# Kernel optimization log

Hardware: AMD Instinct MI355X
Metric: run time of the kernel (lower is better)

## Reference

```python
import jax, jax.numpy as jnp
import numpy as np

LN_EPS = 1e-5  # torch LayerNorm default


def layer_norm(x, g, b):
    m = jnp.mean(x, axis=-1, keepdims=True)
    v = jnp.mean((x - m) ** 2, axis=-1, keepdims=True)
    return (x - m) / jnp.sqrt(v + LN_EPS) * g + b


def scatter_mean(src, idx, n):
    # src: [E, h], idx: [E] -> [n, h], mean with count clamped to >= 1
    s = jax.ops.segment_sum(src, idx, num_segments=n)
    cnt = jax.ops.segment_sum(jnp.ones((src.shape[0],), src.dtype), idx, num_segments=n)
    return s / jnp.clip(cnt, 1.0)[:, None]


def setup_inputs() -> dict:
    key = jax.random.key(0)
    ks = jax.random.split(key, 16)
    N, C, E, h = 200000, 50000, 600000, 128

    def w(k, shape, fan_in):
        return (jax.random.normal(k, shape, jnp.float32) / np.float32(np.sqrt(fan_in)))

    ci = jax.random.randint(ks[2], (E,), 0, C)
    vi = jax.random.randint(ks[3], (E,), 0, N)
    return {
        "vh": jax.random.normal(ks[0], (N, h), jnp.float32),
        "ch": jax.random.normal(ks[1], (C, h), jnp.float32),
        "edge_index": jnp.stack([ci, vi]).astype(jnp.int64),
        "ew": jax.random.normal(ks[4], (E,), jnp.float32),
        "v2c_lin_w": w(ks[5], (h, h), h), "v2c_lin_b": jnp.zeros((h,), jnp.float32),
        "v2c_gate_w": w(ks[6], (h, 1), 1), "v2c_gate_b": jnp.zeros((h,), jnp.float32),
        "v2c_upd_w": w(ks[7], (h, 2 * h), 2 * h), "v2c_upd_b": jnp.zeros((h,), jnp.float32),
        "v2c_ln_g": jnp.ones((h,), jnp.float32), "v2c_ln_b": jnp.zeros((h,), jnp.float32),
        "c2v_lin_w": w(ks[8], (h, h), h), "c2v_lin_b": jnp.zeros((h,), jnp.float32),
        "c2v_gate_w": w(ks[9], (h, 1), 1), "c2v_gate_b": jnp.zeros((h,), jnp.float32),
        "c2v_upd_w": w(ks[10], (h, 2 * h), 2 * h), "c2v_upd_b": jnp.zeros((h,), jnp.float32),
        "c2v_ln_g": jnp.ones((h,), jnp.float32), "c2v_ln_b": jnp.zeros((h,), jnp.float32),
    }


def reference(vh, ch, edge_index, ew,
              v2c_lin_w, v2c_lin_b, v2c_gate_w, v2c_gate_b,
              v2c_upd_w, v2c_upd_b, v2c_ln_g, v2c_ln_b,
              c2v_lin_w, c2v_lin_b, c2v_gate_w, c2v_gate_b,
              c2v_upd_w, c2v_upd_b, c2v_ln_g, c2v_ln_b):
    ci, vi = edge_index[0], edge_index[1]
    e = ew[:, None]  # [E, 1]

    # var -> con
    gate = jax.nn.sigmoid(e @ v2c_gate_w.T + v2c_gate_b)          # [E, h]
    msg = (vh @ v2c_lin_w.T + v2c_lin_b)[vi] * gate               # gather + gate
    agg = scatter_mean(msg, ci, ch.shape[0])                      # [C, h]
    ch_new = jax.nn.relu(layer_norm(
        jnp.concatenate([agg, ch], -1) @ v2c_upd_w.T + v2c_upd_b,
        v2c_ln_g, v2c_ln_b))

    # con -> var (uses updated ch)
    gate = jax.nn.sigmoid(e @ c2v_gate_w.T + c2v_gate_b)
    msg = (ch_new @ c2v_lin_w.T + c2v_lin_b)[ci] * gate
    agg = scatter_mean(msg, vi, vh.shape[0])                      # [N, h]
    vh_new = jax.nn.relu(layer_norm(
        jnp.concatenate([agg, vh], -1) @ c2v_upd_w.T + c2v_upd_b,
        c2v_ln_g, c2v_ln_b))

    return vh_new, ch_new
```

## Files before the change

### kernel.cpp

```cpp
#include <hip/hip_runtime.h>

#define LN_EPS 1e-5f

typedef float f32x4 __attribute__((ext_vector_type(4)));
typedef short bf16x8 __attribute__((ext_vector_type(8)));
typedef unsigned short u16x4 __attribute__((ext_vector_type(4)));

__device__ __forceinline__ unsigned short f2bf(float f) {
  unsigned int u = __float_as_uint(f);
  u = (u + 0x7fffu + ((u >> 16) & 1u)) >> 16;
  return (unsigned short)u;
}
__device__ __forceinline__ float bf2f(unsigned short h) {
  return __uint_as_float((unsigned int)h << 16);
}
__device__ __forceinline__ float sigm(float x) {
  return 1.f / (1.f + __expf(-x));
}

__global__ __launch_bounds__(256) void cvt_hist(const float* __restrict__ wa,
                                                const float* __restrict__ wb,
                                                const float* __restrict__ wc,
                                                const float* __restrict__ wd,
                                                unsigned short* __restrict__ oa,
                                                unsigned short* __restrict__ ob,
                                                unsigned short* __restrict__ oc,
                                                unsigned short* __restrict__ od,
                                                const int* __restrict__ ci,
                                                const int* __restrict__ vi,
                                                int* __restrict__ cntC,
                                                int* __restrict__ cntV,
                                                int* __restrict__ rankC,
                                                int* __restrict__ rankV, int E, int hgrid) {
  if ((int)blockIdx.x < 384) {
    int i = blockIdx.x * 256 + threadIdx.x;
    if (i < 16384) oa[i] = f2bf(wa[i]);
    else if (i < 49152) ob[i - 16384] = f2bf(wb[i - 16384]);
    else if (i < 65536) oc[i - 49152] = f2bf(wc[i - 49152]);
    else if (i < 98304) od[i - 65536] = f2bf(wd[i - 65536]);
    return;
  }
  int hb = blockIdx.x - 384;
  int tid = hb * 256 + threadIdx.x;
  int T = hgrid * 256;
  int e[4], c[4], v[4];
  bool ok[4];
#pragma unroll
  for (int i = 0; i < 4; ++i) {
    e[i] = tid + i * T;
    ok[i] = e[i] < E;
  }
#pragma unroll
  for (int i = 0; i < 4; ++i) if (ok[i]) c[i] = ci[e[i]];
#pragma unroll
  for (int i = 0; i < 4; ++i) if (ok[i]) v[i] = vi[e[i]];
  int rc[4], rv[4];
#pragma unroll
  for (int i = 0; i < 4; ++i) if (ok[i]) rc[i] = atomicAdd(&cntC[c[i]], 1);
#pragma unroll
  for (int i = 0; i < 4; ++i) if (ok[i]) rv[i] = atomicAdd(&cntV[v[i]], 1);
#pragma unroll
  for (int i = 0; i < 4; ++i) if (ok[i]) rankC[e[i]] = rc[i];
#pragma unroll
  for (int i = 0; i < 4; ++i) if (ok[i]) rankV[e[i]] = rv[i];
}

__device__ __forceinline__ void scan1_body(const int* __restrict__ cnt,
                                           int* __restrict__ off,
                                           int* __restrict__ bsum, int M, int bid,
                                           int* s) {
  int base = bid * 1024 + threadIdx.x * 4;
  int v[4];
  int tot = 0;
#pragma unroll
  for (int i = 0; i < 4; ++i) {
    int idx = base + i;
    v[i] = (idx < M) ? cnt[idx] : 0;
    tot += v[i];
  }
  s[threadIdx.x] = tot;
  __syncthreads();
  for (int d = 1; d < 256; d <<= 1) {
    int t = (threadIdx.x >= d) ? s[threadIdx.x - d] : 0;
    __syncthreads();
    s[threadIdx.x] += t;
    __syncthreads();
  }
  int excl = s[threadIdx.x] - tot;
#pragma unroll
  for (int i = 0; i < 4; ++i) {
    int idx = base + i;
    if (idx < M) off[idx] = excl;
    excl += v[i];
  }
  if (threadIdx.x == 255) bsum[bid] = s[255];
}

__global__ __launch_bounds__(256) void scanA(const int* __restrict__ cntC,
                                             int* __restrict__ offC,
                                             int* __restrict__ bsC, int Mc,
                                             const int* __restrict__ cntV,
                                             int* __restrict__ offV,
                                             int* __restrict__ bsV, int Mv, int nbC) {
  __shared__ int s[256];
  if ((int)blockIdx.x < nbC)
    scan1_body(cntC, offC, bsC, Mc, blockIdx.x, s);
  else
    scan1_body(cntV, offV, bsV, Mv, blockIdx.x - nbC, s);
}

__global__ __launch_bounds__(256) void scanB(int* __restrict__ bsC, int nbC,
                                             int* __restrict__ bsV, int nbV) {
  __shared__ int s[256];
  __shared__ int carry;
  int* bsum = (blockIdx.x == 0) ? bsC : bsV;
  int nb = (blockIdx.x == 0) ? nbC : nbV;
  if (threadIdx.x == 0) carry = 0;
  __syncthreads();
  for (int base = 0; base < nb; base += 256) {
    int idx = base + threadIdx.x;
    int v = (idx < nb) ? bsum[idx] : 0;
    s[threadIdx.x] = v;
    __syncthreads();
    for (int d = 1; d < 256; d <<= 1) {
      int t = (threadIdx.x >= d) ? s[threadIdx.x - d] : 0;
      __syncthreads();
      s[threadIdx.x] += t;
      __syncthreads();
    }
    if (idx < nb) bsum[idx] = s[threadIdx.x] - v + carry;
    __syncthreads();
    if (threadIdx.x == 0) carry += s[255];
    __syncthreads();
  }
}

__global__ __launch_bounds__(256) void scanC(int* __restrict__ offC,
                                             const int* __restrict__ bsC, int Mc,
                                             int* __restrict__ offV,
                                             const int* __restrict__ bsV, int Mv,
                                             int E, int gC) {
  if ((int)blockIdx.x < gC) {
    int idx = blockIdx.x * 256 + threadIdx.x;
    if (idx < Mc) offC[idx] += bsC[idx >> 10];
    if (idx == Mc) offC[Mc] = E;
  } else {
    int idx = (blockIdx.x - gC) * 256 + threadIdx.x;
    if (idx < Mv) offV[idx] += bsV[idx >> 10];
    if (idx == Mv) offV[Mv] = E;
  }
}

__global__ __launch_bounds__(512) void lin_scatter(
    const float* __restrict__ X, const unsigned short* __restrict__ Wbf,
    const float* __restrict__ bias, unsigned short* __restrict__ out,
    unsigned short* __restrict__ bfdst, int M,
    const int* __restrict__ ci, const int* __restrict__ vi,
    const float* __restrict__ ew, const int* __restrict__ offC,
    const int* __restrict__ offV, const int* __restrict__ rankC,
    const int* __restrict__ rankV, int2* __restrict__ edataC,
    int2* __restrict__ edataV, int E, int sgrid) {
  __shared__ unsigned short Bs[128][136];
  const int tid = threadIdx.x;
  const int bid = blockIdx.x;
  const int s3 = 3 * sgrid;

  bool isScatter;
  int sidx = 0, lidx;
  if (bid < s3) {
    if (bid % 3 == 0) {
      isScatter = true;
      sidx = bid / 3;
    } else {
      isScatter = false;
      lidx = bid - bid / 3 - 1;
    }
  } else {
    isScatter = false;
    lidx = bid - sgrid;
  }

  if (isScatter) {
    int gtid = sidx * 512 + tid;
    int T = sgrid * 512;
    int e[2], c[2], v[2], wb[2], rc[2], rv[2];
    bool ok[2];
#pragma unroll
    for (int i = 0; i < 2; ++i) {
      e[i] = gtid + i * T;
      ok[i] = e[i] < E;
    }
#pragma unroll
    for (int i = 0; i < 2; ++i) if (ok[i]) c[i] = ci[e[i]];
#pragma unroll
    for (int i = 0; i < 2; ++i) if (ok[i]) v[i] = vi[e[i]];
#pragma unroll
    for (int i = 0; i < 2; ++i) if (ok[i]) wb[i] = __float_as_int(ew[e[i]]);
#pragma unroll
    for (int i = 0; i < 2; ++i) if (ok[i]) rc[i] = rankC[e[i]];
#pragma unroll
    for (int i = 0; i < 2; ++i) if (ok[i]) rv[i] = rankV[e[i]];
#pragma unroll
    for (int i = 0; i < 2; ++i) if (ok[i]) edataC[offC[c[i]] + rc[i]] = make_int2(v[i], wb[i]);
#pragma unroll
    for (int i = 0; i < 2; ++i) if (ok[i]) edataV[offV[v[i]] + rv[i]] = make_int2(c[i], wb[i]);
    return;
  }

  const int lane = tid & 63, wv = tid >> 6;
  const int lr = lane & 15, lg = lane >> 4;
  const int row0 = lidx * 128 + wv * 16;
  const int arow = row0 + lr;
  const bool rowok = arow < M;
  const float* xrow = X + (size_t)arow * 128;

  float4 x0[4], x1[4];
#pragma unroll
  for (int ks = 0; ks < 4; ++ks) {
    int kb = ks * 32 + lg * 8;
    if (rowok) {
      x0[ks] = *reinterpret_cast<const float4*>(xrow + kb);
      x1[ks] = *reinterpret_cast<const float4*>(xrow + kb + 4);
    } else {
      x0[ks] = make_float4(0.f, 0.f, 0.f, 0.f);
      x1[ks] = x0[ks];
    }
  }

#pragma unroll
  for (int it = 0; it < 4; ++it) {
    int q = tid + it * 512;
    int n = q >> 4, kq = (q & 15) * 8;
    *reinterpret_cast<bf16x8*>(&Bs[n][kq]) =
        *reinterpret_cast<const bf16x8*>(&Wbf[(size_t)n * 128 + kq]);
  }

  bf16x8 a[4];
#pragma unroll
  for (int ks = 0; ks < 4; ++ks) {
    a[ks] = (bf16x8){(short)f2bf(x0[ks].x), (short)f2bf(x0[ks].y),
                     (short)f2bf(x0[ks].z), (short)f2bf(x0[ks].w),
                     (short)f2bf(x1[ks].x), (short)f2bf(x1[ks].y),
                     (short)f2bf(x1[ks].z), (short)f2bf(x1[ks].w)};
    if (rowok)
      *reinterpret_cast<bf16x8*>(&bfdst[(size_t)arow * 256 + 128 + ks * 32 + lg * 8]) = a[ks];
  }
  __syncthreads();

  f32x4 acc[8];
#pragma unroll
  for (int nf = 0; nf < 8; ++nf) acc[nf] = (f32x4)(0.f);
#pragma unroll
  for (int ks = 0; ks < 4; ++ks) {
#pragma unroll
    for (int nf = 0; nf < 8; ++nf) {
      bf16x8 b = *reinterpret_cast<const bf16x8*>(&Bs[nf * 16 + lr][ks * 32 + lg * 8]);
      acc[nf] = __builtin_amdgcn_mfma_f32_16x16x32_bf16(a[ks], b, acc[nf], 0, 0, 0);
    }
  }

#pragma unroll
  for (int nf = 0; nf < 8; ++nf) {
    int col = nf * 16 + lr;
    float bv = bias[col];
#pragma unroll
    for (int reg = 0; reg < 4; ++reg) {
      int grow = row0 + lg * 4 + reg;
      if (grow < M) out[(size_t)grow * 256 + col] = f2bf(acc[nf][reg] + bv);
    }
  }
}

__global__ __launch_bounds__(256) void seg_reduce(const int* __restrict__ off,
                                                  const int2* __restrict__ edata,
                                                  const float* __restrict__ gw,
                                                  const float* __restrict__ gb,
                                                  const unsigned short* __restrict__ src,
                                                  int srcStride,
                                                  unsigned short* __restrict__ out,
                                                  int outStride, int M) {
  int seg = blockIdx.x * 4 + (threadIdx.x >> 6);
  if (seg >= M) return;
  int j = threadIdx.x & 63;
  int start = off[seg], end = off[seg + 1];
  float gwa = gw[2 * j], gwb = gw[2 * j + 1];
  float gba = gb[2 * j], gbb = gb[2 * j + 1];
  float a0 = 0.f, a1 = 0.f;
  int p = start;
  for (; p + 4 <= end; p += 4) {
    int2 e0 = edata[p], e1 = edata[p + 1], e2 = edata[p + 2], e3 = edata[p + 3];
    unsigned int v0 = *reinterpret_cast<const unsigned int*>(&src[(size_t)e0.x * srcStride + 2 * j]);
    unsigned int v1 = *reinterpret_cast<const unsigned int*>(&src[(size_t)e1.x * srcStride + 2 * j]);
    unsigned int v2 = *reinterpret_cast<const unsigned int*>(&src[(size_t)e2.x * srcStride + 2 * j]);
    unsigned int v3 = *reinterpret_cast<const unsigned int*>(&src[(size_t)e3.x * srcStride + 2 * j]);
    float w0 = __int_as_float(e0.y), w1 = __int_as_float(e1.y);
    float w2 = __int_as_float(e2.y), w3 = __int_as_float(e3.y);
    a0 += bf2f((unsigned short)(v0 & 0xffff)) * sigm(w0 * gwa + gba)
        + bf2f((unsigned short)(v1 & 0xffff)) * sigm(w1 * gwa + gba)
        + bf2f((unsigned short)(v2 & 0xffff)) * sigm(w2 * gwa + gba)
        + bf2f((unsigned short)(v3 & 0xffff)) * sigm(w3 * gwa + gba);
    a1 += bf2f((unsigned short)(v0 >> 16)) * sigm(w0 * gwb + gbb)
        + bf2f((unsigned short)(v1 >> 16)) * sigm(w1 * gwb + gbb)
        + bf2f((unsigned short)(v2 >> 16)) * sigm(w2 * gwb + gbb)
        + bf2f((unsigned short)(v3 >> 16)) * sigm(w3 * gwb + gbb);
  }
  if (p + 2 <= end) {
    int2 e0 = edata[p], e1 = edata[p + 1];
    unsigned int v0 = *reinterpret_cast<const unsigned int*>(&src[(size_t)e0.x * srcStride + 2 * j]);
    unsigned int v1 = *reinterpret_cast<const unsigned int*>(&src[(size_t)e1.x * srcStride + 2 * j]);
    float w0 = __int_as_float(e0.y), w1 = __int_as_float(e1.y);
    a0 += bf2f((unsigned short)(v0 & 0xffff)) * sigm(w0 * gwa + gba)
        + bf2f((unsigned short)(v1 & 0xffff)) * sigm(w1 * gwa + gba);
    a1 += bf2f((unsigned short)(v0 >> 16)) * sigm(w0 * gwb + gbb)
        + bf2f((unsigned short)(v1 >> 16)) * sigm(w1 * gwb + gbb);
    p += 2;
  }
  if (p < end) {
    int2 e0 = edata[p];
    unsigned int v0 = *reinterpret_cast<const unsigned int*>(&src[(size_t)e0.x * srcStride + 2 * j]);
    float w0 = __int_as_float(e0.y);
    a0 += bf2f((unsigned short)(v0 & 0xffff)) * sigm(w0 * gwa + gba);
    a1 += bf2f((unsigned short)(v0 >> 16)) * sigm(w0 * gwb + gbb);
  }
  int cnt = end - start;
  float inv = 1.f / (float)(cnt > 1 ? cnt : 1);
  unsigned int packed = (unsigned int)f2bf(a0 * inv) | ((unsigned int)f2bf(a1 * inv) << 16);
  *reinterpret_cast<unsigned int*>(&out[(size_t)seg * outStride + 2 * j]) = packed;
}

__global__ __launch_bounds__(512) void gemm_lin_reg(const float* __restrict__ X,
                                                    const unsigned short* __restrict__ Wbf,
                                                    const float* __restrict__ bias,
                                                    unsigned short* __restrict__ out,
                                                    int M) {
  __shared__ unsigned short Bs[128][136];
  const int tid = threadIdx.x;
  const int lane = tid & 63, wv = tid >> 6;
  const int lr = lane & 15, lg = lane >> 4;
  const int row0 = blockIdx.x * 128 + wv * 16;
  const int arow = row0 + lr;
  const bool rowok = arow < M;
  const float* xrow = X + (size_t)arow * 128;

  float4 x0[4], x1[4];
#pragma unroll
  for (int ks = 0; ks < 4; ++ks) {
    int kb = ks * 32 + lg * 8;
    if (rowok) {
      x0[ks] = *reinterpret_cast<const float4*>(xrow + kb);
      x1[ks] = *reinterpret_cast<const float4*>(xrow + kb + 4);
    } else {
      x0[ks] = make_float4(0.f, 0.f, 0.f, 0.f);
      x1[ks] = x0[ks];
    }
  }
#pragma unroll
  for (int it = 0; it < 4; ++it) {
    int q = tid + it * 512;
    int n = q >> 4, kq = (q & 15) * 8;
    *reinterpret_cast<bf16x8*>(&Bs[n][kq]) =
        *reinterpret_cast<const bf16x8*>(&Wbf[(size_t)n * 128 + kq]);
  }
  bf16x8 a[4];
#pragma unroll
  for (int ks = 0; ks < 4; ++ks)
    a[ks] = (bf16x8){(short)f2bf(x0[ks].x), (short)f2bf(x0[ks].y),
                     (short)f2bf(x0[ks].z), (short)f2bf(x0[ks].w),
                     (short)f2bf(x1[ks].x), (short)f2bf(x1[ks].y),
                     (short)f2bf(x1[ks].z), (short)f2bf(x1[ks].w)};
  __syncthreads();

  f32x4 acc[8];
#pragma unroll
  for (int nf = 0; nf < 8; ++nf) acc[nf] = (f32x4)(0.f);
#pragma unroll
  for (int ks = 0; ks < 4; ++ks) {
#pragma unroll
    for (int nf = 0; nf < 8; ++nf) {
      bf16x8 b = *reinterpret_cast<const bf16x8*>(&Bs[nf * 16 + lr][ks * 32 + lg * 8]);
      acc[nf] = __builtin_amdgcn_mfma_f32_16x16x32_bf16(a[ks], b, acc[nf], 0, 0, 0);
    }
  }
#pragma unroll
  for (int nf = 0; nf < 8; ++nf) {
    int col = nf * 16 + lr;
    float bv = bias[col];
#pragma unroll
    for (int reg = 0; reg < 4; ++reg) {
      int grow = row0 + lg * 4 + reg;
      if (grow < M) out[(size_t)grow * 128 + col] = f2bf(acc[nf][reg] + bv);
    }
  }
}

template <bool CAT>
__global__ __launch_bounds__(512) void gemm_upd_reg(const unsigned short* __restrict__ Xa,
                                                    const float* __restrict__ base,
                                                    const unsigned short* __restrict__ Wbf,
                                                    const float* __restrict__ bias,
                                                    const float* __restrict__ lng,
                                                    const float* __restrict__ lnb,
                                                    float* __restrict__ out, int M) {
  __shared__ unsigned short Bs[128][136];
  const int tid = threadIdx.x;
  const int lane = tid & 63, wv = tid >> 6;
  const int lr = lane & 15, lg = lane >> 4;
  const int row0 = blockIdx.x * 128 + wv * 16;
  const int arow = row0 + lr;
  const bool rowok = arow < M;

  bf16x8 a[8];
  if constexpr (CAT) {
    const unsigned short* xr = Xa + (size_t)arow * 256;
#pragma unroll
    for (int ks = 0; ks < 8; ++ks)
      a[ks] = rowok ? *reinterpret_cast<const bf16x8*>(xr + ks * 32 + lg * 8) : (bf16x8)(short)0;
  } else {
    const unsigned short* ar = Xa + (size_t)arow * 128;
#pragma unroll
    for (int ks = 0; ks < 4; ++ks)
      a[ks] = rowok ? *reinterpret_cast<const bf16x8*>(ar + ks * 32 + lg * 8) : (bf16x8)(short)0;
    const float* br = base + (size_t)arow * 128;
#pragma unroll
    for (int ks = 4; ks < 8; ++ks) {
      float4 f0 = make_float4(0.f, 0.f, 0.f, 0.f), f1 = f0;
      if (rowok) {
        int kb = (ks - 4) * 32 + lg * 8;
        f0 = *reinterpret_cast<const float4*>(br + kb);
        f1 = *reinterpret_cast<const float4*>(br + kb + 4);
      }
      a[ks] = (bf16x8){(short)f2bf(f0.x), (short)f2bf(f0.y), (short)f2bf(f0.z), (short)f2bf(f0.w),
                       (short)f2bf(f1.x), (short)f2bf(f1.y), (short)f2bf(f1.z), (short)f2bf(f1.w)};
    }
  }

  auto stageW = [&](int kh) {
#pragma unroll
    for (int it = 0; it < 4; ++it) {
      int q = tid + it * 512;
      int n = q >> 4, kq = (q & 15) * 8;
      *reinterpret_cast<bf16x8*>(&Bs[n][kq]) =
          *reinterpret_cast<const bf16x8*>(&Wbf[(size_t)n * 256 + kh * 128 + kq]);
    }
  };

  f32x4 acc[8];
#pragma unroll
  for (int nf = 0; nf < 8; ++nf) acc[nf] = (f32x4)(0.f);

  stageW(0);
  __syncthreads();
#pragma unroll
  for (int ks = 0; ks < 4; ++ks) {
#pragma unroll
    for (int nf = 0; nf < 8; ++nf) {
      bf16x8 b = *reinterpret_cast<const bf16x8*>(&Bs[nf * 16 + lr][ks * 32 + lg * 8]);
      acc[nf] = __builtin_amdgcn_mfma_f32_16x16x32_bf16(a[ks], b, acc[nf], 0, 0, 0);
    }
  }
  __syncthreads();
  stageW(1);
  __syncthreads();
#pragma unroll
  for (int ks = 4; ks < 8; ++ks) {
#pragma unroll
    for (int nf = 0; nf < 8; ++nf) {
      bf16x8 b = *reinterpret_cast<const bf16x8*>(&Bs[nf * 16 + lr][(ks - 4) * 32 + lg * 8]);
      acc[nf] = __builtin_amdgcn_mfma_f32_16x16x32_bf16(a[ks], b, acc[nf], 0, 0, 0);
    }
  }

  float bv[8], gv[8], lv[8];
#pragma unroll
  for (int nf = 0; nf < 8; ++nf) {
    int col = nf * 16 + lr;
    bv[nf] = bias[col];
    gv[nf] = lng[col];
    lv[nf] = lnb[col];
  }
#pragma unroll
  for (int reg = 0; reg < 4; ++reg) {
    float z[8];
    float s = 0.f, q = 0.f;
#pragma unroll
    for (int nf = 0; nf < 8; ++nf) {
      z[nf] = acc[nf][reg] + bv[nf];
      s += z[nf];
      q += z[nf] * z[nf];
    }
#pragma unroll
    for (int m = 1; m < 16; m <<= 1) {
      s += __shfl_xor(s, m);
      q += __shfl_xor(q, m);
    }
    float mean = s * (1.f / 128.f);
    float var = q * (1.f / 128.f) - mean * mean;
    float rstd = rsqrtf(var + LN_EPS);
    int grow = row0 + lg * 4 + reg;
    if (grow < M) {
#pragma unroll
      for (int nf = 0; nf < 8; ++nf) {
        float y = (z[nf] - mean) * rstd * gv[nf] + lv[nf];
        out[(size_t)grow * 128 + nf * 16 + lr] = fmaxf(y, 0.f);
      }
    }
  }
}

extern "C" void kernel_launch(void* const* d_in, const int* in_sizes, int n_in,
                              void* d_out, int out_size, void* d_ws, size_t ws_size,
                              hipStream_t stream) {
  const float* vh = (const float*)d_in[0];
  const float* ch = (const float*)d_in[1];
  const int* ei = (const int*)d_in[2];
  const float* ew = (const float*)d_in[3];
  const float* v2c_lin_w = (const float*)d_in[4];
  const float* v2c_lin_b = (const float*)d_in[5];
  const float* v2c_gate_w = (const float*)d_in[6];
  const float* v2c_gate_b = (const float*)d_in[7];
  const float* v2c_upd_w = (const float*)d_in[8];
  const float* v2c_upd_b = (const float*)d_in[9];
  const float* v2c_ln_g = (const float*)d_in[10];
  const float* v2c_ln_b = (const float*)d_in[11];
  const float* c2v_lin_w = (const float*)d_in[12];
  const float* c2v_lin_b = (const float*)d_in[13];
  const float* c2v_gate_w = (const float*)d_in[14];
  const float* c2v_gate_b = (const float*)d_in[15];
  const float* c2v_upd_w = (const float*)d_in[16];
  const float* c2v_upd_b = (const float*)d_in[17];
  const float* c2v_ln_g = (const float*)d_in[18];
  const float* c2v_ln_b = (const float*)d_in[19];

  const int N = in_sizes[0] / 128;
  const int C = in_sizes[1] / 128;
  const int E = in_sizes[3];
  const int* ci = ei;
  const int* vi = ei + E;

  unsigned short* Xcat = (unsigned short*)d_ws;
  unsigned short* aggC = Xcat + (size_t)N * 256;
  unsigned short* wbf = aggC + (size_t)C * 128;
  unsigned short* wbfLinV = wbf;
  unsigned short* wbfUpdV = wbf + 16384;
  unsigned short* wbfLinC = wbf + 49152;
  unsigned short* wbfUpdC = wbf + 65536;
  int* offC = (int*)(wbf + 98304);
  int* offV = offC + (C + 1);
  size_t ofs = (size_t)((offV + (N + 1)) - (int*)d_ws);
  ofs = (ofs + 1) & ~(size_t)1;
  int2* edataC = (int2*)((int*)d_ws + ofs);
  int2* edataV = edataC + E;
  int* cntC = (int*)aggC;
  int* cntV = cntC + C;
  int* bsumC = cntV + N;
  int* bsumV = bsumC + 512;
  int* rankC = bsumV + 512;
  int* rankV = rankC + E;

  float* vhNew = (float*)d_out;
  float* chNew = (float*)d_out + (size_t)N * 128;

  const int hgrid = (E + 4 * 256 - 1) / (4 * 256);
  const int sgrid = (E + 2 * 512 - 1) / (2 * 512);
  const int nbC = (C + 1023) / 1024;
  const int nbN = (N + 1023) / 1024;
  const int gC = (C + 1 + 255) / 256;
  const int gN = (N + 1 + 255) / 256;

  hipMemsetAsync(cntC, 0, (size_t)(C + N) * sizeof(int), stream);
  cvt_hist<<<384 + hgrid, 256, 0, stream>>>(v2c_lin_w, v2c_upd_w, c2v_lin_w, c2v_upd_w,
                                            wbfLinV, wbfUpdV, wbfLinC, wbfUpdC,
                                            ci, vi, cntC, cntV, rankC, rankV, E, hgrid);

  scanA<<<nbC + nbN, 256, 0, stream>>>(cntC, offC, bsumC, C, cntV, offV, bsumV, N, nbC);
  scanB<<<2, 256, 0, stream>>>(bsumC, nbC, bsumV, nbN);
  scanC<<<gC + gN, 256, 0, stream>>>(offC, bsumC, C, offV, bsumV, N, E, gC);

  lin_scatter<<<sgrid + (N + 127) / 128, 512, 0, stream>>>(
      vh, wbfLinV, v2c_lin_b, Xcat, Xcat, N,
      ci, vi, ew, offC, offV, rankC, rankV, edataC, edataV, E, sgrid);

  seg_reduce<<<(C + 3) / 4, 256, 0, stream>>>(offC, edataC, v2c_gate_w, v2c_gate_b,
                                              Xcat, 256, aggC, 128, C);
  gemm_upd_reg<false><<<(C + 127) / 128, 512, 0, stream>>>(aggC, ch, wbfUpdV, v2c_upd_b,
                                                           v2c_ln_g, v2c_ln_b, chNew, C);

  unsigned short* tmpC = aggC;
  gemm_lin_reg<<<(C + 127) / 128, 512, 0, stream>>>(chNew, wbfLinC, c2v_lin_b, tmpC, C);
  seg_reduce<<<(N + 3) / 4, 256, 0, stream>>>(offV, edataV, c2v_gate_w, c2v_gate_b,
                                              tmpC, 128, Xcat, 256, N);
  gemm_upd_reg<true><<<(N + 127) / 128, 512, 0, stream>>>(Xcat, nullptr, wbfUpdC,
                                                          c2v_upd_b, c2v_ln_g, c2v_ln_b,
                                                          vhNew, N);
}
```

Baseline: 317.7 us.

## Read GEMM weights directly from global memory instead of staging in LDS

```diff
diff --git a/kernel.cpp b/kernel.cpp
--- a/kernel.cpp
+++ b/kernel.cpp
@@ -151,7 +151,7 @@
   }
 }
 
-__global__ __launch_bounds__(512) void lin_scatter(
+__global__ __launch_bounds__(256) void lin_scatter(
     const float* __restrict__ X, const unsigned short* __restrict__ Wbf,
     const float* __restrict__ bias, unsigned short* __restrict__ out,
     unsigned short* __restrict__ bfdst, int M,
@@ -160,7 +160,6 @@
     const int* __restrict__ offV, const int* __restrict__ rankC,
     const int* __restrict__ rankV, int2* __restrict__ edataC,
     int2* __restrict__ edataV, int E, int sgrid) {
-  __shared__ unsigned short Bs[128][136];
   const int tid = threadIdx.x;
   const int bid = blockIdx.x;
   const int s3 = 3 * sgrid;
@@ -181,8 +180,8 @@
   }
 
   if (isScatter) {
-    int gtid = sidx * 512 + tid;
-    int T = sgrid * 512;
+    int gtid = sidx * 256 + tid;
+    int T = sgrid * 256;
     int e[2], c[2], v[2], wb[2], rc[2], rv[2];
     bool ok[2];
 #pragma unroll
@@ -209,7 +208,7 @@
 
   const int lane = tid & 63, wv = tid >> 6;
   const int lr = lane & 15, lg = lane >> 4;
-  const int row0 = lidx * 128 + wv * 16;
+  const int row0 = lidx * 64 + wv * 16;
   const int arow = row0 + lr;
   const bool rowok = arow < M;
   const float* xrow = X + (size_t)arow * 128;
@@ -226,15 +225,6 @@
       x1[ks] = x0[ks];
     }
   }
-
-#pragma unroll
-  for (int it = 0; it < 4; ++it) {
-    int q = tid + it * 512;
-    int n = q >> 4, kq = (q & 15) * 8;
-    *reinterpret_cast<bf16x8*>(&Bs[n][kq]) =
-        *reinterpret_cast<const bf16x8*>(&Wbf[(size_t)n * 128 + kq]);
-  }
-
   bf16x8 a[4];
 #pragma unroll
   for (int ks = 0; ks < 4; ++ks) {
@@ -245,7 +235,6 @@
     if (rowok)
       *reinterpret_cast<bf16x8*>(&bfdst[(size_t)arow * 256 + 128 + ks * 32 + lg * 8]) = a[ks];
   }
-  __syncthreads();
 
   f32x4 acc[8];
 #pragma unroll
@@ -254,7 +243,8 @@
   for (int ks = 0; ks < 4; ++ks) {
 #pragma unroll
     for (int nf = 0; nf < 8; ++nf) {
-      bf16x8 b = *reinterpret_cast<const bf16x8*>(&Bs[nf * 16 + lr][ks * 32 + lg * 8]);
+      bf16x8 b = *reinterpret_cast<const bf16x8*>(
+          &Wbf[(size_t)(nf * 16 + lr) * 128 + ks * 32 + lg * 8]);
       acc[nf] = __builtin_amdgcn_mfma_f32_16x16x32_bf16(a[ks], b, acc[nf], 0, 0, 0);
     }
   }
@@ -328,16 +318,15 @@
   *reinterpret_cast<unsigned int*>(&out[(size_t)seg * outStride + 2 * j]) = packed;
 }
 
-__global__ __launch_bounds__(512) void gemm_lin_reg(const float* __restrict__ X,
+__global__ __launch_bounds__(256) void gemm_lin_reg(const float* __restrict__ X,
                                                     const unsigned short* __restrict__ Wbf,
                                                     const float* __restrict__ bias,
                                                     unsigned short* __restrict__ out,
                                                     int M) {
-  __shared__ unsigned short Bs[128][136];
   const int tid = threadIdx.x;
   const int lane = tid & 63, wv = tid >> 6;
   const int lr = lane & 15, lg = lane >> 4;
-  const int row0 = blockIdx.x * 128 + wv * 16;
+  const int row0 = blockIdx.x * 64 + wv * 16;
   const int arow = row0 + lr;
   const bool rowok = arow < M;
   const float* xrow = X + (size_t)arow * 128;
@@ -354,13 +343,6 @@
       x1[ks] = x0[ks];
     }
   }
-#pragma unroll
-  for (int it = 0; it < 4; ++it) {
-    int q = tid + it * 512;
-    int n = q >> 4, kq = (q & 15) * 8;
-    *reinterpret_cast<bf16x8*>(&Bs[n][kq]) =
-        *reinterpret_cast<const bf16x8*>(&Wbf[(size_t)n * 128 + kq]);
-  }
   bf16x8 a[4];
 #pragma unroll
   for (int ks = 0; ks < 4; ++ks)
@@ -368,7 +350,6 @@
                      (short)f2bf(x0[ks].z), (short)f2bf(x0[ks].w),
                      (short)f2bf(x1[ks].x), (short)f2bf(x1[ks].y),
                      (short)f2bf(x1[ks].z), (short)f2bf(x1[ks].w)};
-  __syncthreads();
 
   f32x4 acc[8];
 #pragma unroll
@@ -377,7 +358,8 @@
   for (int ks = 0; ks < 4; ++ks) {
 #pragma unroll
     for (int nf = 0; nf < 8; ++nf) {
-      bf16x8 b = *reinterpret_cast<const bf16x8*>(&Bs[nf * 16 + lr][ks * 32 + lg * 8]);
+      bf16x8 b = *reinterpret_cast<const bf16x8*>(
+          &Wbf[(size_t)(nf * 16 + lr) * 128 + ks * 32 + lg * 8]);
       acc[nf] = __builtin_amdgcn_mfma_f32_16x16x32_bf16(a[ks], b, acc[nf], 0, 0, 0);
     }
   }
@@ -394,18 +376,17 @@
 }
 
 template <bool CAT>
-__global__ __launch_bounds__(512) void gemm_upd_reg(const unsigned short* __restrict__ Xa,
+__global__ __launch_bounds__(256) void gemm_upd_reg(const unsigned short* __restrict__ Xa,
                                                     const float* __restrict__ base,
                                                     const unsigned short* __restrict__ Wbf,
                                                     const float* __restrict__ bias,
                                                     const float* __restrict__ lng,
                                                     const float* __restrict__ lnb,
                                                     float* __restrict__ out, int M) {
-  __shared__ unsigned short Bs[128][136];
   const int tid = threadIdx.x;
   const int lane = tid & 63, wv = tid >> 6;
   const int lr = lane & 15, lg = lane >> 4;
-  const int row0 = blockIdx.x * 128 + wv * 16;
+  const int row0 = blockIdx.x * 64 + wv * 16;
   const int arow = row0 + lr;
   const bool rowok = arow < M;
 
@@ -434,38 +415,15 @@
     }
   }
 
-  auto stageW = [&](int kh) {
-#pragma unroll
-    for (int it = 0; it < 4; ++it) {
-      int q = tid + it * 512;
-      int n = q >> 4, kq = (q & 15) * 8;
-      *reinterpret_cast<bf16x8*>(&Bs[n][kq]) =
-          *reinterpret_cast<const bf16x8*>(&Wbf[(size_t)n * 256 + kh * 128 + kq]);
-    }
-  };
-
   f32x4 acc[8];
 #pragma unroll
   for (int nf = 0; nf < 8; ++nf) acc[nf] = (f32x4)(0.f);
-
-  stageW(0);
-  __syncthreads();
-#pragma unroll
-  for (int ks = 0; ks < 4; ++ks) {
+#pragma unroll
+  for (int ks = 0; ks < 8; ++ks) {
 #pragma unroll
     for (int nf = 0; nf < 8; ++nf) {
-      bf16x8 b = *reinterpret_cast<const bf16x8*>(&Bs[nf * 16 + lr][ks * 32 + lg * 8]);
-      acc[nf] = __builtin_amdgcn_mfma_f32_16x16x32_bf16(a[ks], b, acc[nf], 0, 0, 0);
-    }
-  }
-  __syncthreads();
-  stageW(1);
-  __syncthreads();
-#pragma unroll
-  for (int ks = 4; ks < 8; ++ks) {
-#pragma unroll
-    for (int nf = 0; nf < 8; ++nf) {
-      bf16x8 b = *reinterpret_cast<const bf16x8*>(&Bs[nf * 16 + lr][(ks - 4) * 32 + lg * 8]);
+      bf16x8 b = *reinterpret_cast<const bf16x8*>(
+          &Wbf[(size_t)(nf * 16 + lr) * 256 + ks * 32 + lg * 8]);
       acc[nf] = __builtin_amdgcn_mfma_f32_16x16x32_bf16(a[ks], b, acc[nf], 0, 0, 0);
     }
   }
@@ -561,7 +519,7 @@
   float* chNew = (float*)d_out + (size_t)N * 128;
 
   const int hgrid = (E + 4 * 256 - 1) / (4 * 256);
-  const int sgrid = (E + 2 * 512 - 1) / (2 * 512);
+  const int sgrid = (E + 2 * 256 - 1) / (2 * 256);
   const int nbC = (C + 1023) / 1024;
   const int nbN = (N + 1023) / 1024;
   const int gC = (C + 1 + 255) / 256;
@@ -576,20 +534,20 @@
   scanB<<<2, 256, 0, stream>>>(bsumC, nbC, bsumV, nbN);
   scanC<<<gC + gN, 256, 0, stream>>>(offC, bsumC, C, offV, bsumV, N, E, gC);
 
-  lin_scatter<<<sgrid + (N + 127) / 128, 512, 0, stream>>>(
+  lin_scatter<<<sgrid + (N + 63) / 64, 256, 0, stream>>>(
       vh, wbfLinV, v2c_lin_b, Xcat, Xcat, N,
       ci, vi, ew, offC, offV, rankC, rankV, edataC, edataV, E, sgrid);
 
   seg_reduce<<<(C + 3) / 4, 256, 0, stream>>>(offC, edataC, v2c_gate_w, v2c_gate_b,
                                               Xcat, 256, aggC, 128, C);
-  gemm_upd_reg<false><<<(C + 127) / 128, 512, 0, stream>>>(aggC, ch, wbfUpdV, v2c_upd_b,
-                                                           v2c_ln_g, v2c_ln_b, chNew, C);
+  gemm_upd_reg<false><<<(C + 63) / 64, 256, 0, stream>>>(aggC, ch, wbfUpdV, v2c_upd_b,
+                                                         v2c_ln_g, v2c_ln_b, chNew, C);
 
   unsigned short* tmpC = aggC;
-  gemm_lin_reg<<<(C + 127) / 128, 512, 0, stream>>>(chNew, wbfLinC, c2v_lin_b, tmpC, C);
+  gemm_lin_reg<<<(C + 63) / 64, 256, 0, stream>>>(chNew, wbfLinC, c2v_lin_b, tmpC, C);
   seg_reduce<<<(N + 3) / 4, 256, 0, stream>>>(offV, edataV, c2v_gate_w, c2v_gate_b,
                                               tmpC, 128, Xcat, 256, N);
-  gemm_upd_reg<true><<<(N + 127) / 128, 512, 0, stream>>>(Xcat, nullptr, wbfUpdC,
-                                                          c2v_upd_b, c2v_ln_g, c2v_ln_b,
-                                                          vhNew, N);
-}
+  gemm_upd_reg<true><<<(N + 63) / 64, 256, 0, stream>>>(Xcat, nullptr, wbfUpdC,
+                                                        c2v_upd_b, c2v_ln_g, c2v_ln_b,
+                                                        vhNew, N);
+}
```

Result: slower. 462.2 us (+45.5%).
